# Kernel optimization log

Measured on AMD Instinct MI355X. Metric: run time of the kernel, lower is better.

The kernel has to match this reference:

```python
import jax, jax.numpy as jnp
import numpy as np

EMBED_DIMS = 1024
NUM_HEADS = 16
HEAD_DIMS = EMBED_DIMS // NUM_HEADS


def setup_inputs() -> dict:
    key = jax.random.key(0)
    k_x, k_wqkv, k_bqkv, k_wp, k_bp = jax.random.split(key, 5)
    B, N, D = 2, 2048, EMBED_DIMS
    x = jax.random.normal(k_x, (B, N, D), dtype=jnp.float32)
    # torch nn.Linear(in, out): weight [out, in], y = x @ W.T + b
    s = 1.0 / np.sqrt(D)
    W_qkv = jax.random.uniform(k_wqkv, (3 * D, D), jnp.float32, -s, s)
    b_qkv = jax.random.uniform(k_bqkv, (3 * D,), jnp.float32, -s, s)
    W_proj = jax.random.uniform(k_wp, (D, D), jnp.float32, -s, s)
    b_proj = jax.random.uniform(k_bp, (D,), jnp.float32, -s, s)
    return {"x": x, "W_qkv": W_qkv, "b_qkv": b_qkv, "W_proj": W_proj, "b_proj": b_proj}


def reference(x, W_qkv, b_qkv, W_proj, b_proj):
    B, N, D = x.shape
    H, Hd = NUM_HEADS, HEAD_DIMS
    # qkv projection: [B, N, 3, H, Hd] -> split q, k, v as [B, H, N, Hd]
    qkv = (x @ W_qkv.T + b_qkv).reshape(B, N, 3, H, Hd).transpose(2, 0, 3, 1, 4)
    q, k, v = qkv[0], qkv[1], qkv[2]
    scale = 1.0 / jnp.sqrt(jnp.asarray(Hd, x.dtype))
    attn = jnp.einsum("bhqd,bhkd->bhqk", q, k) * scale  # [B, H, N, N]
    attn = jax.nn.softmax(attn, axis=-1)
    out = jnp.einsum("bhqk,bhkd->bhqd", attn, v)  # [B, H, N, Hd]
    out = out.transpose(0, 2, 1, 3).reshape(B, N, D)
    out = out @ W_proj.T + b_proj
    return out
```

## Files before the change

### kernel.cpp

```cpp
#include <hip/hip_runtime.h>

typedef _Float16 f16x8 __attribute__((ext_vector_type(8)));
typedef __attribute__((ext_vector_type(4))) float f32x4;

static __device__ __forceinline__ unsigned short f2h(float f) {
  return __builtin_bit_cast(unsigned short, (_Float16)f);
}

#if __has_builtin(__builtin_amdgcn_exp2f)
#define EXP2(x) __builtin_amdgcn_exp2f(x)
#else
#define EXP2(x) exp2f(x)
#endif

#define GLOAD_LDS16(gp, lp)                                          \
  __builtin_amdgcn_global_load_lds(                                  \
      (const __attribute__((address_space(1))) unsigned int*)(gp),   \
      (__attribute__((address_space(3))) unsigned int*)(lp), 16, 0, 0)

__global__ __launch_bounds__(256) void cvt_all(
    const float* __restrict__ X, const float* __restrict__ Wq,
    const float* __restrict__ Wp, unsigned short* __restrict__ Xb,
    unsigned short* __restrict__ Wqb, unsigned short* __restrict__ Wpb) {
  const int i = blockIdx.x * 256 + threadIdx.x;
  const float4* src;
  unsigned short* dst;
  int off;
  if (i < 1048576) {
    src = (const float4*)X; dst = Xb; off = i;
  } else if (i < 1835008) {
    src = (const float4*)Wq; dst = Wqb; off = i - 1048576;
  } else {
    src = (const float4*)Wp; dst = Wpb; off = i - 1835008;
  }
  const float4 v = src[off];
  *(ushort4*)(dst + (size_t)off * 4) =
      make_ushort4(f2h(v.x), f2h(v.y), f2h(v.z), f2h(v.w));
}

__global__ __launch_bounds__(256) void qkv_gemm(
    const unsigned short* __restrict__ Xb, const unsigned short* __restrict__ Wb,
    const float* __restrict__ bias, unsigned short* __restrict__ Qb,
    unsigned short* __restrict__ Kb, unsigned short* __restrict__ Vt) {
  __shared__ __align__(16) unsigned short A_sh[128 * 32];
  __shared__ __align__(16) unsigned short B_sh[128 * 32];
  const int n0 = blockIdx.x * 128, m0 = blockIdx.y * 128;
  const int tid = threadIdx.x, lane = tid & 63, wave = tid >> 6;
  const int wr = wave >> 1, wc = wave & 1, lm = lane & 15, lg = lane >> 4;
  const int lrow = lane >> 2, lcol = (lane & 3) * 8;

  f32x4 acc[4][4] = {};

  for (int k0 = 0; k0 < 1024; k0 += 32) {
#pragma unroll
    for (int j = 0; j < 2; ++j) {
      const int chunk = wave * 2 + j;
      const int row = chunk * 16 + lrow;
      GLOAD_LDS16(Xb + (size_t)(m0 + row) * 1024 + k0 + lcol, &A_sh[chunk * 512]);
      GLOAD_LDS16(Wb + (size_t)(n0 + row) * 1024 + k0 + lcol, &B_sh[chunk * 512]);
    }
    __syncthreads();
    f16x8 af[4], bfr[4];
#pragma unroll
    for (int mi = 0; mi < 4; ++mi)
      af[mi] = *(const f16x8*)&A_sh[(wr * 64 + mi * 16 + lm) * 32 + lg * 8];
#pragma unroll
    for (int ni = 0; ni < 4; ++ni)
      bfr[ni] = *(const f16x8*)&B_sh[(wc * 64 + ni * 16 + lm) * 32 + lg * 8];
#pragma unroll
    for (int mi = 0; mi < 4; ++mi)
#pragma unroll
      for (int ni = 0; ni < 4; ++ni)
        acc[mi][ni] = __builtin_amdgcn_mfma_f32_16x16x32_f16(
            af[mi], bfr[ni], acc[mi][ni], 0, 0, 0);
    __syncthreads();
  }

  const float qscale = 0.18033688011112042f;
#pragma unroll
  for (int mi = 0; mi < 4; ++mi) {
#pragma unroll
    for (int ni = 0; ni < 4; ++ni) {
      const int gn = n0 + wc * 64 + ni * 16 + lm;
      const float bv = bias[gn];
      const int which = gn >> 10;
      const int h = (gn >> 6) & 15;
      const int hd = gn & 63;
      float v[4];
#pragma unroll
      for (int r = 0; r < 4; ++r) v[r] = acc[mi][ni][r] + bv;
      const int gm0 = m0 + wr * 64 + mi * 16 + lg * 4;
      const int bb = gm0 >> 11;
      const int nq0 = gm0 & 2047;
      if (which == 0) {
        unsigned short* p = Qb + (((size_t)bb * 16 + h) * 2048 + nq0) * 64 + hd;
        p[0] = f2h(v[0] * qscale);   p[64] = f2h(v[1] * qscale);
        p[128] = f2h(v[2] * qscale); p[192] = f2h(v[3] * qscale);
      } else if (which == 1) {
        unsigned short* p = Kb + (((size_t)bb * 16 + h) * 2048 + nq0) * 64 + hd;
        p[0] = f2h(v[0]);   p[64] = f2h(v[1]);
        p[128] = f2h(v[2]); p[192] = f2h(v[3]);
      } else {
        *(ushort4*)(Vt + (((size_t)bb * 16 + h) * 64 + hd) * 2048 + nq0) =
            make_ushort4(f2h(v[0]), f2h(v[1]), f2h(v[2]), f2h(v[3]));
      }
    }
  }
}

__global__ __launch_bounds__(512) void attn_kernel(
    const unsigned short* __restrict__ Qb, const unsigned short* __restrict__ Kb,
    const unsigned short* __restrict__ Vt, unsigned short* __restrict__ Ob) {
  __shared__ __align__(16) unsigned short K_sh[2][2][64 * 32];
  __shared__ __align__(16) unsigned short V_sh[2][2][64 * 32];
  __shared__ __align__(16) unsigned short P_sh[128 * 68];
  const int bh = blockIdx.y, q0 = blockIdx.x * 128;
  const size_t base = (size_t)bh * (2048 * 64);
  const unsigned short* Qp = Qb + base;
  const unsigned short* Kp = Kb + base;
  const unsigned short* Vp = Vt + base;
  const int tid = threadIdx.x, lane = tid & 63, wave = tid >> 6;
  const int lm = lane & 15, lg = lane >> 4;
  const int r4 = lane >> 2;
  const int sg8 = (((lane & 3) ^ ((r4 >> 1) & 3)) * 8);
  const int lgx = (lg ^ ((lm >> 1) & 3)) * 8;

  f16x8 qf[2];
#pragma unroll
  for (int kc = 0; kc < 2; ++kc)
    qf[kc] = *(const f16x8*)(Qp +
        (size_t)(q0 + wave * 16 + lm) * 64 + kc * 32 + lg * 8);

  f32x4 o[4] = {};
  float lsum[4] = {};

  const bool isV = wave >= 4;
  const int plane = wave & 1;
  const int half = (wave >> 1) & 1;

#define STAGE(kt_, b_)                                                        \
  do {                                                                        \
    if (!isV) {                                                               \
      _Pragma("unroll")                                                       \
      for (int qv = 0; qv < 2; ++qv)                                          \
        GLOAD_LDS16(Kp + (size_t)((kt_) * 64 + half * 32 + qv * 16 + r4) * 64 \
                        + plane * 32 + sg8,                                   \
                    &K_sh[b_][plane][(half * 2 + qv) * 512]);                 \
    } else {                                                                  \
      _Pragma("unroll")                                                       \
      for (int qv = 0; qv < 2; ++qv)                                          \
        GLOAD_LDS16(Vp + (size_t)(half * 32 + qv * 16 + r4) * 2048 +          \
                        (kt_) * 64 + plane * 32 + sg8,                        \
                    &V_sh[b_][plane][(half * 2 + qv) * 512]);                 \
    }                                                                         \
  } while (0)

  STAGE(0, 0);

  for (int kt = 0; kt < 32; ++kt) {
    const int cur = kt & 1;
    __syncthreads();
    if (kt < 31) STAGE(kt + 1, cur ^ 1);

    f32x4 s[4] = {};
#pragma unroll
    for (int kc = 0; kc < 2; ++kc) {
#pragma unroll
      for (int ni = 0; ni < 4; ++ni) {
        const f16x8 kf =
            *(const f16x8*)&K_sh[cur][kc][(ni * 16 + lm) * 32 + lgx];
        s[ni] = __builtin_amdgcn_mfma_f32_16x16x32_f16(qf[kc], kf, s[ni], 0, 0, 0);
      }
    }

#pragma unroll
    for (int ni = 0; ni < 4; ++ni) {
      float p0 = EXP2(s[ni][0]), p1 = EXP2(s[ni][1]);
      float p2 = EXP2(s[ni][2]), p3 = EXP2(s[ni][3]);
      lsum[0] += p0; lsum[1] += p1; lsum[2] += p2; lsum[3] += p3;
      unsigned short* pp = &P_sh[(wave * 16 + lg * 4) * 68 + ni * 16 + lm];
      pp[0] = f2h(p0);    pp[68] = f2h(p1);
      pp[136] = f2h(p2);  pp[204] = f2h(p3);
    }

#pragma unroll
    for (int kc = 0; kc < 2; ++kc) {
      const f16x8 pa =
          *(const f16x8*)&P_sh[(wave * 16 + lm) * 68 + kc * 32 + lg * 8];
#pragma unroll
      for (int ni = 0; ni < 4; ++ni) {
        const f16x8 vb =
            *(const f16x8*)&V_sh[cur][kc][(ni * 16 + lm) * 32 + lgx];
        o[ni] = __builtin_amdgcn_mfma_f32_16x16x32_f16(pa, vb, o[ni], 0, 0, 0);
      }
    }
  }
#undef STAGE

  const int b = bh >> 4, h = bh & 15;
#pragma unroll
  for (int r = 0; r < 4; ++r) {
    float l = lsum[r];
    l += __shfl_xor(l, 1);
    l += __shfl_xor(l, 2);
    l += __shfl_xor(l, 4);
    l += __shfl_xor(l, 8);
    const float inv = 1.0f / l;
    const int nq = q0 + wave * 16 + lg * 4 + r;
    unsigned short* p = Ob + ((size_t)(b * 2048 + nq) * 16 + h) * 64 + lm;
    p[0] = f2h(o[0][r] * inv);
    p[16] = f2h(o[1][r] * inv);
    p[32] = f2h(o[2][r] * inv);
    p[48] = f2h(o[3][r] * inv);
  }
}

__global__ __launch_bounds__(256) void proj_gemm(
    const unsigned short* __restrict__ A, const unsigned short* __restrict__ Wb,
    const float* __restrict__ bias, float* __restrict__ Out) {
  __shared__ __align__(16) unsigned short A_sh[64 * 32];
  __shared__ __align__(16) unsigned short B_sh[128 * 32];
  const int n0 = blockIdx.x * 128, m0 = blockIdx.y * 64;
  const int tid = threadIdx.x, lane = tid & 63, wave = tid >> 6;
  const int wr = wave >> 1, wc = wave & 1, lm = lane & 15, lg = lane >> 4;
  const int lrow = lane >> 2, lcol = (lane & 3) * 8;

  f32x4 acc[2][4] = {};

  for (int k0 = 0; k0 < 1024; k0 += 32) {
    {
      const int row = wave * 16 + lrow;
      GLOAD_LDS16(A + (size_t)(m0 + row) * 1024 + k0 + lcol, &A_sh[wave * 512]);
    }
#pragma unroll
    for (int j = 0; j < 2; ++j) {
      const int chunk = wave * 2 + j;
      const int row = chunk * 16 + lrow;
      GLOAD_LDS16(Wb + (size_t)(n0 + row) * 1024 + k0 + lcol, &B_sh[chunk * 512]);
    }
    __syncthreads();
    f16x8 af[2], bfr[4];
#pragma unroll
    for (int mi = 0; mi < 2; ++mi)
      af[mi] = *(const f16x8*)&A_sh[(wr * 32 + mi * 16 + lm) * 32 + lg * 8];
#pragma unroll
    for (int ni = 0; ni < 4; ++ni)
      bfr[ni] = *(const f16x8*)&B_sh[(wc * 64 + ni * 16 + lm) * 32 + lg * 8];
#pragma unroll
    for (int mi = 0; mi < 2; ++mi)
#pragma unroll
      for (int ni = 0; ni < 4; ++ni)
        acc[mi][ni] = __builtin_amdgcn_mfma_f32_16x16x32_f16(
            af[mi], bfr[ni], acc[mi][ni], 0, 0, 0);
    __syncthreads();
  }

#pragma unroll
  for (int mi = 0; mi < 2; ++mi)
#pragma unroll
    for (int ni = 0; ni < 4; ++ni) {
      const int gn = n0 + wc * 64 + ni * 16 + lm;
      const float bv = bias[gn];
#pragma unroll
      for (int r = 0; r < 4; ++r) {
        const int gm = m0 + wr * 32 + mi * 16 + lg * 4 + r;
        Out[(size_t)gm * 1024 + gn] = acc[mi][ni][r] + bv;
      }
    }
}

extern "C" void kernel_launch(void* const* d_in, const int* in_sizes, int n_in,
                              void* d_out, int out_size, void* d_ws, size_t ws_size,
                              hipStream_t stream) {
  const float* x      = (const float*)d_in[0];
  const float* W_qkv  = (const float*)d_in[1];
  const float* b_qkv  = (const float*)d_in[2];
  const float* W_proj = (const float*)d_in[3];
  const float* b_proj = (const float*)d_in[4];
  float* out = (float*)d_out;

  unsigned short* Qb  = (unsigned short*)d_ws;
  unsigned short* Kb  = Qb + 4194304;
  unsigned short* Vt  = Kb + 4194304;
  unsigned short* Ao  = Vt + 4194304;
  unsigned short* Xb  = Ao + 4194304;
  unsigned short* Wqb = Xb + 4194304;
  unsigned short* Wpb = Wqb + 3145728;

  cvt_all<<<8192, 256, 0, stream>>>(x, W_qkv, W_proj, Xb, Wqb, Wpb);
  qkv_gemm<<<dim3(24, 32), 256, 0, stream>>>(Xb, Wqb, b_qkv, Qb, Kb, Vt);
  attn_kernel<<<dim3(16, 32), 512, 0, stream>>>(Qb, Kb, Vt, Ao);
  proj_gemm<<<dim3(8, 64), 256, 0, stream>>>(Ao, Wpb, b_proj, out);
}
```

Measured before the change: 193.0 us.

## Double-buffer LDS tiles and XOR-swizzle columns in QKV and projection GEMMs

Both GEMM kernels now keep two LDS buffers and issue the global-to-LDS loads for the next K-slice before computing on the current one, so there is one barrier per iteration instead of two. The goal is to overlap global-memory latency with MFMA work. The 16-byte column chunk within each row is also XOR-swizzled with a row-derived key on store and on fragment read, to cut LDS bank conflicts. In exchange the kernels use twice the shared memory, which may lower occupancy. Correctness also depends on the swizzle being applied the same way on both sides and on the barrier placement being safe for buffer reuse.

```diff
diff --git a/kernel.cpp b/kernel.cpp
--- a/kernel.cpp
+++ b/kernel.cpp
@@ -42,39 +42,52 @@
     const unsigned short* __restrict__ Xb, const unsigned short* __restrict__ Wb,
     const float* __restrict__ bias, unsigned short* __restrict__ Qb,
     unsigned short* __restrict__ Kb, unsigned short* __restrict__ Vt) {
-  __shared__ __align__(16) unsigned short A_sh[128 * 32];
-  __shared__ __align__(16) unsigned short B_sh[128 * 32];
+  __shared__ __align__(16) unsigned short A_sh[2][128 * 32];
+  __shared__ __align__(16) unsigned short B_sh[2][128 * 32];
   const int n0 = blockIdx.x * 128, m0 = blockIdx.y * 128;
   const int tid = threadIdx.x, lane = tid & 63, wave = tid >> 6;
   const int wr = wave >> 1, wc = wave & 1, lm = lane & 15, lg = lane >> 4;
-  const int lrow = lane >> 2, lcol = (lane & 3) * 8;
+  const int r4 = lane >> 2;
+  const int sg8 = (((lane & 3) ^ ((r4 >> 1) & 3)) * 8);
+  const int lgx = (lg ^ ((lm >> 1) & 3)) * 8;
 
   f32x4 acc[4][4] = {};
 
-  for (int k0 = 0; k0 < 1024; k0 += 32) {
-#pragma unroll
-    for (int j = 0; j < 2; ++j) {
-      const int chunk = wave * 2 + j;
-      const int row = chunk * 16 + lrow;
-      GLOAD_LDS16(Xb + (size_t)(m0 + row) * 1024 + k0 + lcol, &A_sh[chunk * 512]);
-      GLOAD_LDS16(Wb + (size_t)(n0 + row) * 1024 + k0 + lcol, &B_sh[chunk * 512]);
-    }
+#define QSTAGE(k0_, b_)                                                       \
+  do {                                                                        \
+    _Pragma("unroll")                                                         \
+    for (int j = 0; j < 2; ++j) {                                             \
+      const int chunk = wave * 2 + j;                                         \
+      const int row = chunk * 16 + r4;                                        \
+      GLOAD_LDS16(Xb + (size_t)(m0 + row) * 1024 + (k0_) + sg8,               \
+                  &A_sh[b_][chunk * 512]);                                    \
+      GLOAD_LDS16(Wb + (size_t)(n0 + row) * 1024 + (k0_) + sg8,               \
+                  &B_sh[b_][chunk * 512]);                                    \
+    }                                                                         \
+  } while (0)
+
+  QSTAGE(0, 0);
+
+  for (int it = 0; it < 32; ++it) {
+    const int cur = it & 1;
     __syncthreads();
+    if (it < 31) QSTAGE((it + 1) * 32, cur ^ 1);
+
     f16x8 af[4], bfr[4];
 #pragma unroll
     for (int mi = 0; mi < 4; ++mi)
-      af[mi] = *(const f16x8*)&A_sh[(wr * 64 + mi * 16 + lm) * 32 + lg * 8];
+      af[mi] = *(const f16x8*)&A_sh[cur][(wr * 64 + mi * 16 + lm) * 32 + lgx];
 #pragma unroll
     for (int ni = 0; ni < 4; ++ni)
-      bfr[ni] = *(const f16x8*)&B_sh[(wc * 64 + ni * 16 + lm) * 32 + lg * 8];
+      bfr[ni] = *(const f16x8*)&B_sh[cur][(wc * 64 + ni * 16 + lm) * 32 + lgx];
 #pragma unroll
     for (int mi = 0; mi < 4; ++mi)
 #pragma unroll
       for (int ni = 0; ni < 4; ++ni)
         acc[mi][ni] = __builtin_amdgcn_mfma_f32_16x16x32_f16(
             af[mi], bfr[ni], acc[mi][ni], 0, 0, 0);
-    __syncthreads();
-  }
+  }
+#undef QSTAGE
 
   const float qscale = 0.18033688011112042f;
 #pragma unroll
@@ -218,42 +231,55 @@
 __global__ __launch_bounds__(256) void proj_gemm(
     const unsigned short* __restrict__ A, const unsigned short* __restrict__ Wb,
     const float* __restrict__ bias, float* __restrict__ Out) {
-  __shared__ __align__(16) unsigned short A_sh[64 * 32];
-  __shared__ __align__(16) unsigned short B_sh[128 * 32];
+  __shared__ __align__(16) unsigned short A_sh[2][64 * 32];
+  __shared__ __align__(16) unsigned short B_sh[2][128 * 32];
   const int n0 = blockIdx.x * 128, m0 = blockIdx.y * 64;
   const int tid = threadIdx.x, lane = tid & 63, wave = tid >> 6;
   const int wr = wave >> 1, wc = wave & 1, lm = lane & 15, lg = lane >> 4;
-  const int lrow = lane >> 2, lcol = (lane & 3) * 8;
+  const int r4 = lane >> 2;
+  const int sg8 = (((lane & 3) ^ ((r4 >> 1) & 3)) * 8);
+  const int lgx = (lg ^ ((lm >> 1) & 3)) * 8;
 
   f32x4 acc[2][4] = {};
 
-  for (int k0 = 0; k0 < 1024; k0 += 32) {
-    {
-      const int row = wave * 16 + lrow;
-      GLOAD_LDS16(A + (size_t)(m0 + row) * 1024 + k0 + lcol, &A_sh[wave * 512]);
-    }
-#pragma unroll
-    for (int j = 0; j < 2; ++j) {
-      const int chunk = wave * 2 + j;
-      const int row = chunk * 16 + lrow;
-      GLOAD_LDS16(Wb + (size_t)(n0 + row) * 1024 + k0 + lcol, &B_sh[chunk * 512]);
-    }
+#define PSTAGE(k0_, b_)                                                       \
+  do {                                                                        \
+    {                                                                         \
+      const int row = wave * 16 + r4;                                         \
+      GLOAD_LDS16(A + (size_t)(m0 + row) * 1024 + (k0_) + sg8,                \
+                  &A_sh[b_][wave * 512]);                                     \
+    }                                                                         \
+    _Pragma("unroll")                                                         \
+    for (int j = 0; j < 2; ++j) {                                             \
+      const int chunk = wave * 2 + j;                                         \
+      const int row = chunk * 16 + r4;                                        \
+      GLOAD_LDS16(Wb + (size_t)(n0 + row) * 1024 + (k0_) + sg8,               \
+                  &B_sh[b_][chunk * 512]);                                    \
+    }                                                                         \
+  } while (0)
+
+  PSTAGE(0, 0);
+
+  for (int it = 0; it < 32; ++it) {
+    const int cur = it & 1;
     __syncthreads();
+    if (it < 31) PSTAGE((it + 1) * 32, cur ^ 1);
+
     f16x8 af[2], bfr[4];
 #pragma unroll
     for (int mi = 0; mi < 2; ++mi)
-      af[mi] = *(const f16x8*)&A_sh[(wr * 32 + mi * 16 + lm) * 32 + lg * 8];
+      af[mi] = *(const f16x8*)&A_sh[cur][(wr * 32 + mi * 16 + lm) * 32 + lgx];
 #pragma unroll
     for (int ni = 0; ni < 4; ++ni)
-      bfr[ni] = *(const f16x8*)&B_sh[(wc * 64 + ni * 16 + lm) * 32 + lg * 8];
+      bfr[ni] = *(const f16x8*)&B_sh[cur][(wc * 64 + ni * 16 + lm) * 32 + lgx];
 #pragma unroll
     for (int mi = 0; mi < 2; ++mi)
 #pragma unroll
       for (int ni = 0; ni < 4; ++ni)
         acc[mi][ni] = __builtin_amdgcn_mfma_f32_16x16x32_f16(
             af[mi], bfr[ni], acc[mi][ni], 0, 0, 0);
-    __syncthreads();
-  }
+  }
+#undef PSTAGE
 
 #pragma unroll
   for (int mi = 0; mi < 2; ++mi)
```

Measured after the change: 197.2 us. 2.1% more time.

## Fuse fp32-to-fp16 conversion into GEMM tile loads and enlarge proj tile

Applied to the files above, without the earlier changes.

Removes the separate conversion kernel and instead loads fp32 X and weights directly in the QKV and projection GEMMs, converting to fp16 while staging into padded LDS. This drops one launch and the round trip of writing and re-reading the fp16 copies. In exchange, the async global-to-LDS loads become synchronous register loads with per-tile conversion, and each tile reads twice the bytes from global memory. The weights are also converted repeatedly by every block that uses them. The projection GEMM tile also grows from 64 to 128 rows, which halves its grid.

```diff
diff --git a/kernel.cpp b/kernel.cpp
--- a/kernel.cpp
+++ b/kernel.cpp
@@ -18,55 +18,39 @@
       (const __attribute__((address_space(1))) unsigned int*)(gp),   \
       (__attribute__((address_space(3))) unsigned int*)(lp), 16, 0, 0)
 
-__global__ __launch_bounds__(256) void cvt_all(
-    const float* __restrict__ X, const float* __restrict__ Wq,
-    const float* __restrict__ Wp, unsigned short* __restrict__ Xb,
-    unsigned short* __restrict__ Wqb, unsigned short* __restrict__ Wpb) {
-  const int i = blockIdx.x * 256 + threadIdx.x;
-  const float4* src;
-  unsigned short* dst;
-  int off;
-  if (i < 1048576) {
-    src = (const float4*)X; dst = Xb; off = i;
-  } else if (i < 1835008) {
-    src = (const float4*)Wq; dst = Wqb; off = i - 1048576;
-  } else {
-    src = (const float4*)Wp; dst = Wpb; off = i - 1835008;
-  }
-  const float4 v = src[off];
-  *(ushort4*)(dst + (size_t)off * 4) =
-      make_ushort4(f2h(v.x), f2h(v.y), f2h(v.z), f2h(v.w));
-}
-
 __global__ __launch_bounds__(256) void qkv_gemm(
-    const unsigned short* __restrict__ Xb, const unsigned short* __restrict__ Wb,
+    const float* __restrict__ X, const float* __restrict__ W,
     const float* __restrict__ bias, unsigned short* __restrict__ Qb,
     unsigned short* __restrict__ Kb, unsigned short* __restrict__ Vt) {
-  __shared__ __align__(16) unsigned short A_sh[128 * 32];
-  __shared__ __align__(16) unsigned short B_sh[128 * 32];
+  __shared__ unsigned short A_sh[128][40];
+  __shared__ unsigned short B_sh[128][40];
   const int n0 = blockIdx.x * 128, m0 = blockIdx.y * 128;
   const int tid = threadIdx.x, lane = tid & 63, wave = tid >> 6;
   const int wr = wave >> 1, wc = wave & 1, lm = lane & 15, lg = lane >> 4;
-  const int lrow = lane >> 2, lcol = (lane & 3) * 8;
 
   f32x4 acc[4][4] = {};
 
   for (int k0 = 0; k0 < 1024; k0 += 32) {
 #pragma unroll
-    for (int j = 0; j < 2; ++j) {
-      const int chunk = wave * 2 + j;
-      const int row = chunk * 16 + lrow;
-      GLOAD_LDS16(Xb + (size_t)(m0 + row) * 1024 + k0 + lcol, &A_sh[chunk * 512]);
-      GLOAD_LDS16(Wb + (size_t)(n0 + row) * 1024 + k0 + lcol, &B_sh[chunk * 512]);
+    for (int i = 0; i < 4; ++i) {
+      const int c = tid + 256 * i;
+      const int row = c >> 3;
+      const int col = (c & 7) << 2;
+      const float4 va = *(const float4*)(X + (size_t)(m0 + row) * 1024 + k0 + col);
+      const float4 vb = *(const float4*)(W + (size_t)(n0 + row) * 1024 + k0 + col);
+      *(ushort4*)&A_sh[row][col] =
+          make_ushort4(f2h(va.x), f2h(va.y), f2h(va.z), f2h(va.w));
+      *(ushort4*)&B_sh[row][col] =
+          make_ushort4(f2h(vb.x), f2h(vb.y), f2h(vb.z), f2h(vb.w));
     }
     __syncthreads();
     f16x8 af[4], bfr[4];
 #pragma unroll
     for (int mi = 0; mi < 4; ++mi)
-      af[mi] = *(const f16x8*)&A_sh[(wr * 64 + mi * 16 + lm) * 32 + lg * 8];
+      af[mi] = *(const f16x8*)&A_sh[wr * 64 + mi * 16 + lm][lg * 8];
 #pragma unroll
     for (int ni = 0; ni < 4; ++ni)
-      bfr[ni] = *(const f16x8*)&B_sh[(wc * 64 + ni * 16 + lm) * 32 + lg * 8];
+      bfr[ni] = *(const f16x8*)&B_sh[wc * 64 + ni * 16 + lm][lg * 8];
 #pragma unroll
     for (int mi = 0; mi < 4; ++mi)
 #pragma unroll
@@ -216,38 +200,44 @@
 }
 
 __global__ __launch_bounds__(256) void proj_gemm(
-    const unsigned short* __restrict__ A, const unsigned short* __restrict__ Wb,
+    const unsigned short* __restrict__ A, const float* __restrict__ W,
     const float* __restrict__ bias, float* __restrict__ Out) {
-  __shared__ __align__(16) unsigned short A_sh[64 * 32];
-  __shared__ __align__(16) unsigned short B_sh[128 * 32];
-  const int n0 = blockIdx.x * 128, m0 = blockIdx.y * 64;
+  __shared__ unsigned short A_sh[128][40];
+  __shared__ unsigned short B_sh[128][40];
+  const int n0 = blockIdx.x * 128, m0 = blockIdx.y * 128;
   const int tid = threadIdx.x, lane = tid & 63, wave = tid >> 6;
   const int wr = wave >> 1, wc = wave & 1, lm = lane & 15, lg = lane >> 4;
-  const int lrow = lane >> 2, lcol = (lane & 3) * 8;
-
-  f32x4 acc[2][4] = {};
+
+  f32x4 acc[4][4] = {};
 
   for (int k0 = 0; k0 < 1024; k0 += 32) {
-    {
-      const int row = wave * 16 + lrow;
-      GLOAD_LDS16(A + (size_t)(m0 + row) * 1024 + k0 + lcol, &A_sh[wave * 512]);
-    }
-#pragma unroll
-    for (int j = 0; j < 2; ++j) {
-      const int chunk = wave * 2 + j;
-      const int row = chunk * 16 + lrow;
-      GLOAD_LDS16(Wb + (size_t)(n0 + row) * 1024 + k0 + lcol, &B_sh[chunk * 512]);
-    }
-    __syncthreads();
-    f16x8 af[2], bfr[4];
-#pragma unroll
-    for (int mi = 0; mi < 2; ++mi)
-      af[mi] = *(const f16x8*)&A_sh[(wr * 32 + mi * 16 + lm) * 32 + lg * 8];
+#pragma unroll
+    for (int i = 0; i < 2; ++i) {
+      const int c = tid + 256 * i;
+      const int row = c >> 2;
+      const int col = (c & 3) << 3;
+      *(uint4*)&A_sh[row][col] =
+          *(const uint4*)(A + (size_t)(m0 + row) * 1024 + k0 + col);
+    }
+#pragma unroll
+    for (int i = 0; i < 4; ++i) {
+      const int c = tid + 256 * i;
+      const int row = c >> 3;
+      const int col = (c & 7) << 2;
+      const float4 vb = *(const float4*)(W + (size_t)(n0 + row) * 1024 + k0 + col);
+      *(ushort4*)&B_sh[row][col] =
+          make_ushort4(f2h(vb.x), f2h(vb.y), f2h(vb.z), f2h(vb.w));
+    }
+    __syncthreads();
+    f16x8 af[4], bfr[4];
+#pragma unroll
+    for (int mi = 0; mi < 4; ++mi)
+      af[mi] = *(const f16x8*)&A_sh[wr * 64 + mi * 16 + lm][lg * 8];
 #pragma unroll
     for (int ni = 0; ni < 4; ++ni)
-      bfr[ni] = *(const f16x8*)&B_sh[(wc * 64 + ni * 16 + lm) * 32 + lg * 8];
-#pragma unroll
-    for (int mi = 0; mi < 2; ++mi)
+      bfr[ni] = *(const f16x8*)&B_sh[wc * 64 + ni * 16 + lm][lg * 8];
+#pragma unroll
+    for (int mi = 0; mi < 4; ++mi)
 #pragma unroll
       for (int ni = 0; ni < 4; ++ni)
         acc[mi][ni] = __builtin_amdgcn_mfma_f32_16x16x32_f16(
@@ -256,14 +246,14 @@
   }
 
 #pragma unroll
-  for (int mi = 0; mi < 2; ++mi)
+  for (int mi = 0; mi < 4; ++mi)
 #pragma unroll
     for (int ni = 0; ni < 4; ++ni) {
       const int gn = n0 + wc * 64 + ni * 16 + lm;
       const float bv = bias[gn];
 #pragma unroll
       for (int r = 0; r < 4; ++r) {
-        const int gm = m0 + wr * 32 + mi * 16 + lg * 4 + r;
+        const int gm = m0 + wr * 64 + mi * 16 + lg * 4 + r;
         Out[(size_t)gm * 1024 + gn] = acc[mi][ni][r] + bv;
       }
     }
@@ -279,16 +269,12 @@
   const float* b_proj = (const float*)d_in[4];
   float* out = (float*)d_out;
 
-  unsigned short* Qb  = (unsigned short*)d_ws;
-  unsigned short* Kb  = Qb + 4194304;
-  unsigned short* Vt  = Kb + 4194304;
-  unsigned short* Ao  = Vt + 4194304;
-  unsigned short* Xb  = Ao + 4194304;
-  unsigned short* Wqb = Xb + 4194304;
-  unsigned short* Wpb = Wqb + 3145728;
-
-  cvt_all<<<8192, 256, 0, stream>>>(x, W_qkv, W_proj, Xb, Wqb, Wpb);
-  qkv_gemm<<<dim3(24, 32), 256, 0, stream>>>(Xb, Wqb, b_qkv, Qb, Kb, Vt);
+  unsigned short* Qb = (unsigned short*)d_ws;
+  unsigned short* Kb = Qb + 4194304;
+  unsigned short* Vt = Kb + 4194304;
+  unsigned short* Ao = Vt + 4194304;
+
+  qkv_gemm<<<dim3(24, 32), 256, 0, stream>>>(x, W_qkv, b_qkv, Qb, Kb, Vt);
   attn_kernel<<<dim3(16, 32), 512, 0, stream>>>(Qb, Kb, Vt, Ao);
-  proj_gemm<<<dim3(8, 64), 256, 0, stream>>>(Ao, Wpb, b_proj, out);
-}
+  proj_gemm<<<dim3(8, 32), 256, 0, stream>>>(Ao, W_proj, b_proj, out);
+}
```

After: 218.5 us. 1.13x slower.
